# Kernel optimization log

Hardware: AMD Instinct MI355X
Metric: run time of the kernel (lower is better)

The kernel has to match this reference:

```python
import jax, jax.numpy as jnp
import numpy as np

B, C, H, W = 64, 512, 64, 64
RED = 16
HID = C // RED  # 32
N_EXPERTS = 3

def setup_inputs() -> dict:
    key = jax.random.key(0)
    k1, k2, k3, k4 = jax.random.split(key, 4)
    x = jax.random.normal(k1, (B, C, H, W), dtype=jnp.float32)
    dataset = jax.random.randint(k2, (B,), 0, N_EXPERTS, dtype=jnp.int32)
    # torch Linear weight layout: [out_features, in_features]
    W1 = jax.random.normal(k3, (N_EXPERTS, HID, C), dtype=jnp.float32) * (1.0 / np.sqrt(C))
    W2 = jax.random.normal(k4, (N_EXPERTS, C, HID), dtype=jnp.float32) * (1.0 / np.sqrt(HID))
    return {"x": x, "dataset": dataset, "W1": W1, "W2": W2}

def reference(x, dataset, W1, W2):
    # global average pool: [B, C]
    y = jnp.mean(x, axis=(2, 3))
    # per-sample expert weights, routed by dataset id
    w1 = W1[dataset]  # [B, HID, C]
    w2 = W2[dataset]  # [B, C, HID]
    h = jax.nn.relu(jnp.einsum('bc,bhc->bh', y, w1))
    gate = jax.nn.sigmoid(jnp.einsum('bh,bch->bc', h, w2))  # [B, C]
    return x * gate[:, :, None, None]
```

## Files before the change

kernel.cpp:

```cpp
#include <hip/hip_runtime.h>
#include <math.h>

#define NB 64
#define NC 512
#define NHW 4096
#define NHID 32
#define NPLANES (NB * NC)

typedef float f32x4 __attribute__((ext_vector_type(4)));

__global__ __launch_bounds__(256) void pool_kernel(const float* __restrict__ x,
                                                   float* __restrict__ y) {
    const int wid   = threadIdx.x >> 6;
    const int lane  = threadIdx.x & 63;
    const int plane = blockIdx.x * 4 + wid;
    const f32x4* __restrict__ xin =
        reinterpret_cast<const f32x4*>(x + (size_t)plane * NHW);

    float s = 0.f;
#pragma unroll
    for (int i = 0; i < 16; ++i) {
        f32x4 v = xin[lane + i * 64];
        s += v.x + v.y + v.z + v.w;
    }
#pragma unroll
    for (int o = 32; o; o >>= 1) s += __shfl_down(s, o, 64);
    if (lane == 0) y[plane] = s * (1.0f / NHW);
}

__global__ __launch_bounds__(256) void gate_kernel(const float* __restrict__ y,
                                                   const int* __restrict__ dataset,
                                                   const float* __restrict__ W1,
                                                   const float* __restrict__ W2,
                                                   float* __restrict__ gate) {
    const int b = blockIdx.x;
    const int tid = threadIdx.x;

    __shared__ float ys[NC];
    __shared__ float hs[NHID];

    ys[tid]       = y[b * NC + tid];
    ys[tid + 256] = y[b * NC + tid + 256];
    const int e = dataset[b];
    __syncthreads();

    const int hid = tid >> 3;
    const int j   = tid & 7;
    const float* __restrict__ w1row = W1 + ((size_t)e * NHID + hid) * NC;
    float acc = 0.f;
    for (int c = j; c < NC; c += 8) acc += ys[c] * w1row[c];
#pragma unroll
    for (int o = 4; o; o >>= 1) acc += __shfl_down(acc, o, 8);
    if (j == 0) hs[hid] = fmaxf(acc, 0.f);
    __syncthreads();

    const float* __restrict__ w2base = W2 + (size_t)e * NC * NHID;
#pragma unroll
    for (int k = 0; k < 2; ++k) {
        const int c = tid + k * 256;
        const float* __restrict__ w2row = w2base + c * NHID;
        float z = 0.f;
#pragma unroll
        for (int hh = 0; hh < NHID; ++hh) z += hs[hh] * w2row[hh];
        gate[b * NC + c] = 1.0f / (1.0f + expf(-z));
    }
}

__global__ __launch_bounds__(256) void scale_kernel(const float* __restrict__ x,
                                                    const float* __restrict__ gate,
                                                    float* __restrict__ out) {
    const int blk = gridDim.x - 1 - blockIdx.x;
    const int p0 = blk * 4;
    const size_t base = (size_t)blk * 4096;
    const f32x4* __restrict__ xin = reinterpret_cast<const f32x4*>(x);
    f32x4* __restrict__ o4 = reinterpret_cast<f32x4*>(out);
    const int t = threadIdx.x;

    float g[4];
#pragma unroll
    for (int q = 0; q < 4; ++q) g[q] = gate[p0 + q];

    f32x4 v[16];
#pragma unroll
    for (int q = 0; q < 4; ++q)
#pragma unroll
        for (int k = 0; k < 4; ++k)
            v[q * 4 + k] = xin[base + (size_t)q * 1024 + k * 256 + t];

#pragma unroll
    for (int q = 0; q < 4; ++q)
#pragma unroll
        for (int k = 0; k < 4; ++k) {
            f32x4 w = v[q * 4 + k] * g[q];
            __builtin_nontemporal_store(w, &o4[base + (size_t)q * 1024 + k * 256 + t]);
        }
}

extern "C" void kernel_launch(void* const* d_in, const int* in_sizes, int n_in,
                              void* d_out, int out_size, void* d_ws, size_t ws_size,
                              hipStream_t stream) {
    const float* x       = (const float*)d_in[0];
    const int*   dataset = (const int*)d_in[1];
    const float* W1      = (const float*)d_in[2];
    const float* W2      = (const float*)d_in[3];
    float* out = (float*)d_out;

    float* y    = (float*)d_ws;
    float* gate = y + NB * NC;

    pool_kernel<<<NPLANES / 4, 256, 0, stream>>>(x, y);
    gate_kernel<<<NB, 256, 0, stream>>>(y, dataset, W1, W2, gate);
    scale_kernel<<<NPLANES / 4, 256, 0, stream>>>(x, gate, out);
}
```

Before: 289.1 us.

## Fuse pool, gate and scale into one persistent kernel with grid barriers

Replaces the three-kernel pipeline with one persistent kernel of 256 blocks. Each block owns two channels and walks the batch in chunks of 8 samples, keeping its slice of x in registers. Per chunk it pools, meets the other blocks at a global atomic barrier, recomputes the gate MLP for its channels, and scales and writes out. The goal is to read x from HBM once instead of twice and to remove launch gaps. The cost is 8 grid-wide barriers, redundant per-block MLP work, a memset for the barrier counters, and reliance on all 256 blocks being resident at once.

After: 1.119 ms. 287% more time.

```diff
diff --git a/kernel.cpp b/kernel.cpp
--- a/kernel.cpp
+++ b/kernel.cpp
@@ -5,95 +5,127 @@
 #define NC 512
 #define NHW 4096
 #define NHID 32
-#define NPLANES (NB * NC)
+#define GRID 256
+#define BLK 512
+#define CHUNK 8
+#define NCHUNKS (NB / CHUNK)
 
 typedef float f32x4 __attribute__((ext_vector_type(4)));
 
-__global__ __launch_bounds__(256) void pool_kernel(const float* __restrict__ x,
-                                                   float* __restrict__ y) {
-    const int wid   = threadIdx.x >> 6;
-    const int lane  = threadIdx.x & 63;
-    const int plane = blockIdx.x * 4 + wid;
-    const f32x4* __restrict__ xin =
-        reinterpret_cast<const f32x4*>(x + (size_t)plane * NHW);
-
-    float s = 0.f;
-#pragma unroll
-    for (int i = 0; i < 16; ++i) {
-        f32x4 v = xin[lane + i * 64];
-        s += v.x + v.y + v.z + v.w;
+__device__ __forceinline__ void gbar(unsigned* cnt, unsigned* rel, unsigned k) {
+    __threadfence();
+    __syncthreads();
+    if (threadIdx.x == 0) {
+        unsigned old = atomicAdd(cnt, 1u);
+        if (old == k * GRID - 1u) {
+            __hip_atomic_store(rel, k, __ATOMIC_RELEASE, __HIP_MEMORY_SCOPE_AGENT);
+        } else {
+            while (__hip_atomic_load(rel, __ATOMIC_ACQUIRE,
+                                     __HIP_MEMORY_SCOPE_AGENT) < k) {
+                __builtin_amdgcn_s_sleep(2);
+            }
+        }
     }
-#pragma unroll
-    for (int o = 32; o; o >>= 1) s += __shfl_down(s, o, 64);
-    if (lane == 0) y[plane] = s * (1.0f / NHW);
+    __syncthreads();
 }
 
-__global__ __launch_bounds__(256) void gate_kernel(const float* __restrict__ y,
-                                                   const int* __restrict__ dataset,
-                                                   const float* __restrict__ W1,
-                                                   const float* __restrict__ W2,
-                                                   float* __restrict__ gate) {
-    const int b = blockIdx.x;
-    const int tid = threadIdx.x;
+__global__ __launch_bounds__(BLK, 2) void fused_kernel(
+        const float* __restrict__ x,
+        const int* __restrict__ dataset,
+        const float* __restrict__ W1,
+        const float* __restrict__ W2,
+        float* __restrict__ out,
+        float* __restrict__ y,
+        unsigned* __restrict__ cnt,
+        unsigned* __restrict__ rel) {
+    const int tid  = threadIdx.x;
+    const int blk  = blockIdx.x;
+    const int half = tid >> 8;
+    const int l256 = tid & 255;
+    const int wid  = tid >> 6;
+    const int lane = tid & 63;
+    const int c0   = blk * 2;
 
-    __shared__ float ys[NC];
-    __shared__ float hs[NHID];
+    __shared__ float ysl[CHUNK * NC];
+    __shared__ float hsl[CHUNK * NHID];
+    __shared__ float gsl[CHUNK * 2];
+    __shared__ float part[8][CHUNK];
+    __shared__ int   esl[CHUNK];
 
-    ys[tid]       = y[b * NC + tid];
-    ys[tid + 256] = y[b * NC + tid + 256];
-    const int e = dataset[b];
-    __syncthreads();
+    const f32x4* __restrict__ x4 = reinterpret_cast<const f32x4*>(x);
+    f32x4* __restrict__ o4 = reinterpret_cast<f32x4*>(out);
 
-    const int hid = tid >> 3;
-    const int j   = tid & 7;
-    const float* __restrict__ w1row = W1 + ((size_t)e * NHID + hid) * NC;
-    float acc = 0.f;
-    for (int c = j; c < NC; c += 8) acc += ys[c] * w1row[c];
+    for (int ci = 0; ci < NCHUNKS; ++ci) {
+        const int b0 = ci * CHUNK;
+
+        f32x4 v[CHUNK][4];
+        size_t pbase[CHUNK];
 #pragma unroll
-    for (int o = 4; o; o >>= 1) acc += __shfl_down(acc, o, 8);
-    if (j == 0) hs[hid] = fmaxf(acc, 0.f);
-    __syncthreads();
+        for (int s = 0; s < CHUNK; ++s) {
+            pbase[s] = (((size_t)(b0 + s) * NC + c0 + half) << 10) + l256;
+#pragma unroll
+            for (int k = 0; k < 4; ++k)
+                v[s][k] = x4[pbase[s] + (k << 8)];
+        }
+#pragma unroll
+        for (int s = 0; s < CHUNK; ++s) {
+            f32x4 a = v[s][0] + v[s][1] + v[s][2] + v[s][3];
+            float t = a.x + a.y + a.z + a.w;
+#pragma unroll
+            for (int o = 32; o; o >>= 1) t += __shfl_down(t, o, 64);
+            if (lane == 0) part[wid][s] = t;
+        }
+        __syncthreads();
+        if (tid < CHUNK * 2) {
+            const int s = tid >> 1, h = tid & 1;
+            float t = part[h * 4 + 0][s] + part[h * 4 + 1][s] +
+                      part[h * 4 + 2][s] + part[h * 4 + 3][s];
+            y[(b0 + s) * NC + c0 + h] = t * (1.0f / NHW);
+        }
 
-    const float* __restrict__ w2base = W2 + (size_t)e * NC * NHID;
+        gbar(cnt, rel, (unsigned)(ci + 1));
+
+        if (tid < CHUNK) esl[tid] = dataset[b0 + tid];
+        for (int i = tid; i < CHUNK * NC; i += BLK) {
+            const int s = i >> 9, c = i & (NC - 1);
+            ysl[i] = __hip_atomic_load(&y[(b0 + s) * NC + c],
+                                       __ATOMIC_RELAXED, __HIP_MEMORY_SCOPE_AGENT);
+        }
+        __syncthreads();
+        {
+            const int hid = tid >> 4, j = tid & 15;
+            for (int s = 0; s < CHUNK; ++s) {
+                const float* __restrict__ w1row =
+                    W1 + ((size_t)esl[s] * NHID + hid) * NC;
+                float acc = 0.f;
+                for (int c = j; c < NC; c += 16) acc += ysl[s * NC + c] * w1row[c];
 #pragma unroll
-    for (int k = 0; k < 2; ++k) {
-        const int c = tid + k * 256;
-        const float* __restrict__ w2row = w2base + c * NHID;
-        float z = 0.f;
+                for (int o = 8; o; o >>= 1) acc += __shfl_down(acc, o, 16);
+                if (j == 0) hsl[s * NHID + hid] = fmaxf(acc, 0.f);
+            }
+        }
+        __syncthreads();
+        if (tid < CHUNK * 2) {
+            const int s = tid >> 1, ch = tid & 1;
+            const float* __restrict__ w2row =
+                W2 + ((size_t)esl[s] * NC + c0 + ch) * NHID;
+            float z = 0.f;
 #pragma unroll
-        for (int hh = 0; hh < NHID; ++hh) z += hs[hh] * w2row[hh];
-        gate[b * NC + c] = 1.0f / (1.0f + expf(-z));
-    }
-}
-
-__global__ __launch_bounds__(256) void scale_kernel(const float* __restrict__ x,
-                                                    const float* __restrict__ gate,
-                                                    float* __restrict__ out) {
-    const int blk = gridDim.x - 1 - blockIdx.x;
-    const int p0 = blk * 4;
-    const size_t base = (size_t)blk * 4096;
-    const f32x4* __restrict__ xin = reinterpret_cast<const f32x4*>(x);
-    f32x4* __restrict__ o4 = reinterpret_cast<f32x4*>(out);
-    const int t = threadIdx.x;
-
-    float g[4];
-#pragma unroll
-    for (int q = 0; q < 4; ++q) g[q] = gate[p0 + q];
-
-    f32x4 v[16];
-#pragma unroll
-    for (int q = 0; q < 4; ++q)
-#pragma unroll
-        for (int k = 0; k < 4; ++k)
-            v[q * 4 + k] = xin[base + (size_t)q * 1024 + k * 256 + t];
+            for (int h = 0; h < NHID; ++h) z += hsl[s * NHID + h] * w2row[h];
+            gsl[tid] = 1.0f / (1.0f + expf(-z));
+        }
+        __syncthreads();
 
 #pragma unroll
-    for (int q = 0; q < 4; ++q)
+        for (int s = 0; s < CHUNK; ++s) {
+            const float g = gsl[s * 2 + half];
 #pragma unroll
-        for (int k = 0; k < 4; ++k) {
-            f32x4 w = v[q * 4 + k] * g[q];
-            __builtin_nontemporal_store(w, &o4[base + (size_t)q * 1024 + k * 256 + t]);
+            for (int k = 0; k < 4; ++k) {
+                f32x4 w = v[s][k] * g;
+                __builtin_nontemporal_store(w, &o4[pbase[s] + (k << 8)]);
+            }
         }
+    }
 }
 
 extern "C" void kernel_launch(void* const* d_in, const int* in_sizes, int n_in,
@@ -105,10 +137,10 @@
     const float* W2      = (const float*)d_in[3];
     float* out = (float*)d_out;
 
-    float* y    = (float*)d_ws;
-    float* gate = y + NB * NC;
+    unsigned* cnt = (unsigned*)d_ws;
+    unsigned* rel = cnt + 1;
+    float*    y   = (float*)((char*)d_ws + 256);
 
-    pool_kernel<<<NPLANES / 4, 256, 0, stream>>>(x, y);
-    gate_kernel<<<NB, 256, 0, stream>>>(y, dataset, W1, W2, gate);
-    scale_kernel<<<NPLANES / 4, 256, 0, stream>>>(x, gate, out);
+    hipMemsetAsync(d_ws, 0, 256, stream);
+    fused_kernel<<<GRID, BLK, 0, stream>>>(x, dataset, W1, W2, out, y, cnt, rel);
 }
```
